# Kernel optimization log

Hardware: AMD Instinct MI355X
Metric: run time of the kernel (lower is better)

The kernel has to match this reference:

```python
import jax, jax.numpy as jnp
import numpy as np

B, N, C, H = 2, 2048, 1024, 16
D = C // H  # head_dim = 64


def _rope_freqs(n, d_half, theta=10000.0):
    inv = 1.0 / (theta ** (np.arange(0, d_half, dtype=np.float32) / d_half))
    ang = np.arange(n, dtype=np.float32)[:, None] * inv[None, :]
    return jnp.asarray(np.cos(ang)), jnp.asarray(np.sin(ang))


def setup_inputs() -> dict:
    key = jax.random.key(0)
    ks = jax.random.split(key, 5)
    cos, sin = _rope_freqs(N, D // 2)
    s = 0.02
    return {
        "x": jax.random.normal(ks[0], (B, N, C), jnp.float32),
        "w_qkv": jax.random.normal(ks[1], (3 * C, C), jnp.float32) * s,
        "b_qkv": jnp.zeros((3 * C,), jnp.float32),
        "w_proj": jax.random.normal(ks[2], (C, C), jnp.float32) * s,
        "b_proj": jnp.zeros((C,), jnp.float32),
        "freqs_cos": cos,
        "freqs_sin": sin,
    }


def _apply_rope(t, cos, sin):
    # t: (B, H, N, D); consecutive pairs (even, odd) form complex numbers,
    # matching torch.view_as_complex on reshape(..., D//2, 2).
    te = t[..., 0::2]
    to = t[..., 1::2]
    cos = cos[None, None, :, :]  # (1,1,N,D//2)
    sin = sin[None, None, :, :]
    oe = te * cos - to * sin
    oo = te * sin + to * cos
    return jnp.stack([oe, oo], axis=-1).reshape(t.shape)


def reference(x, w_qkv, b_qkv, w_proj, b_proj, freqs_cos, freqs_sin):
    b, n, c = x.shape
    qkv = x @ w_qkv.T + b_qkv                      # (B,N,3C)
    qkv = qkv.reshape(b, n, 3, H, D).transpose(2, 0, 3, 1, 4)  # (3,B,H,N,D)
    q, k, v = qkv[0], qkv[1], qkv[2]
    q = _apply_rope(q, freqs_cos, freqs_sin)
    k = _apply_rope(k, freqs_cos, freqs_sin)
    scale = 1.0 / jnp.sqrt(jnp.asarray(D, x.dtype))
    scores = jnp.einsum("bhqd,bhkd->bhqk", q, k) * scale
    attn = jax.nn.softmax(scores, axis=-1)
    out = jnp.einsum("bhqk,bhkd->bhqd", attn, v)   # (B,H,N,D)
    out = out.transpose(0, 2, 1, 3).reshape(b, n, c)
    return out @ w_proj.T + b_proj
```

## Files before the change

### kernel.cpp

```cpp
#include <hip/hip_runtime.h>
#include <hip/hip_bf16.h>
#include <stdint.h>

#define BB 2
#define NN 2048
#define CC 1024
#define HH 16
#define DD 64
#define C3 3072

typedef __attribute__((ext_vector_type(8))) short bf16x8;
typedef __attribute__((ext_vector_type(4))) float f32x4;
typedef __attribute__((ext_vector_type(4))) unsigned short ushort4_t;

__device__ __forceinline__ unsigned short f2bf(float f) {
  union { float f; unsigned u; } v; v.f = f;
  unsigned r = v.u + 0x7FFFu + ((v.u >> 16) & 1u);
  return (unsigned short)(r >> 16);
}

#if __has_builtin(__builtin_amdgcn_exp2f)
#define EXP2(x) __builtin_amdgcn_exp2f(x)
#else
#define EXP2(x) exp2f(x)
#endif

#define QSCALE 0.18033688f

#define GLDS(g, l) __builtin_amdgcn_global_load_lds( \
    (const __attribute__((address_space(1))) void*)(g), \
    (__attribute__((address_space(3))) void*)(l), 16, 0, 0)

__global__ __launch_bounds__(256) void k_cvt(
    const float* __restrict__ x, const float* __restrict__ wq,
    const float* __restrict__ wp,
    unsigned short* __restrict__ xb, unsigned short* __restrict__ wqb,
    unsigned short* __restrict__ wpb)
{
  int blk = blockIdx.x;
  const float* s; unsigned short* d; int i;
  if (blk < 4096)      { s = x;  d = xb;  i = blk * 256 + threadIdx.x; }
  else if (blk < 7168) { s = wq; d = wqb; i = (blk - 4096) * 256 + threadIdx.x; }
  else                 { s = wp; d = wpb; i = (blk - 7168) * 256 + threadIdx.x; }
  float4 v = ((const float4*)s)[i];
  ushort4_t o;
  o.x = f2bf(v.x); o.y = f2bf(v.y); o.z = f2bf(v.z); o.w = f2bf(v.w);
  ((ushort4_t*)d)[i] = o;
}

__global__ __launch_bounds__(256) void k_gemm_qkv(
    const unsigned short* __restrict__ A, const unsigned short* __restrict__ Bt,
    const float* __restrict__ bias,
    const float* __restrict__ cosb, const float* __restrict__ sinb,
    unsigned short* __restrict__ Qg, unsigned short* __restrict__ Kg,
    unsigned short* __restrict__ Vnd)
{
  __shared__ __align__(16) unsigned short As[128 * 32];
  __shared__ __align__(16) unsigned short Bs[128 * 32];
  const int tid  = threadIdx.x;
  const int lane = tid & 63;
  const int wave = tid >> 6;
  const int bm = blockIdx.y * 128;
  const int bn = blockIdx.x * 128;
  const int wm = (wave >> 1) * 64;
  const int wn = (wave & 1) * 64;
  const int frow = lane & 15;
  const int fk   = (lane >> 4) * 8;
  const int K = 1024;

  f32x4 acc[4][4] = {};

  const int row0 = tid >> 2, cc0 = tid & 3;
  const int row1 = row0 + 64;

  for (int k0 = 0; k0 < K; k0 += 32) {
    GLDS(A  + (size_t)(bm + row0) * K + k0 + cc0 * 8, As + (size_t)tid * 8);
    GLDS(Bt + (size_t)(bn + row0) * K + k0 + cc0 * 8, Bs + (size_t)tid * 8);
    GLDS(A  + (size_t)(bm + row1) * K + k0 + cc0 * 8, As + (size_t)(tid + 256) * 8);
    GLDS(Bt + (size_t)(bn + row1) * K + k0 + cc0 * 8, Bs + (size_t)(tid + 256) * 8);
    __syncthreads();

    bf16x8 af[4], bfr[4];
#pragma unroll
    for (int t = 0; t < 4; ++t) {
      af[t]  = *(const bf16x8*)(As + (wm + t * 16 + frow) * 32 + fk);
      bfr[t] = *(const bf16x8*)(Bs + (wn + t * 16 + frow) * 32 + fk);
    }
#pragma unroll
    for (int mt = 0; mt < 4; ++mt)
#pragma unroll
      for (int nt = 0; nt < 4; ++nt)
        acc[mt][nt] = __builtin_amdgcn_mfma_f32_16x16x32_bf16(af[mt], bfr[nt], acc[mt][nt], 0, 0, 0);
    __syncthreads();
  }

  const int er0  = (lane >> 4) * 4;
  const int ecol = lane & 15;
  const int region = bn >> 10;
  unsigned short* dstQK = (region == 0) ? Qg : Kg;

#pragma unroll
  for (int nt = 0; nt < 4; ++nt) {
    const int col = bn + wn + nt * 16 + ecol;
    const float bv = bias[col];
    const int c64 = (wn + nt * 16 + ecol) & 63;
    const int h   = (col >> 6) & 15;
    const int ii  = c64 >> 1;
#pragma unroll
    for (int mt = 0; mt < 4; ++mt)
#pragma unroll
      for (int r = 0; r < 4; ++r) {
        const int rowg = bm + wm + mt * 16 + er0 + r;
        const int b = rowg >> 11, n = rowg & (NN - 1);
        float v = acc[mt][nt][r] + bv;
        float vp = __shfl_xor(v, 1, 64);
        const size_t o = ((size_t)(b * HH + h) * NN + n) * DD + c64;
        if (region == 2) {
          Vnd[o] = f2bf(v);
        } else {
          float cth = cosb[n * 32 + ii], sth = sinb[n * 32 + ii];
          float ov = (c64 & 1) ? (vp * sth + v * cth)
                               : (v * cth - vp * sth);
          if (region == 0) ov *= QSCALE;
          dstQK[o] = f2bf(ov);
        }
      }
  }
}

__global__ __launch_bounds__(256) void k_vt(
    const unsigned short* __restrict__ Vnd, unsigned short* __restrict__ Vt)
{
  __shared__ unsigned short t[64][66];
  const int tid = threadIdx.x;
  const int bh = blockIdx.x >> 5;
  const int n0 = (blockIdx.x & 31) * 64;

  const unsigned short* src = Vnd + ((size_t)bh * NN + n0) * DD;
  const int nl = tid >> 2, d0 = (tid & 3) * 16;
#pragma unroll
  for (int j = 0; j < 4; ++j) {
    ushort4_t v = *(const ushort4_t*)(src + (size_t)nl * DD + d0 + j * 4);
    t[nl][d0 + j * 4 + 0] = v.x;
    t[nl][d0 + j * 4 + 1] = v.y;
    t[nl][d0 + j * 4 + 2] = v.z;
    t[nl][d0 + j * 4 + 3] = v.w;
  }
  __syncthreads();
  const int d = tid >> 2, m0 = (tid & 3) * 16;
  unsigned short* dst = Vt + ((size_t)bh * DD + d) * NN + n0 + m0;
#pragma unroll
  for (int j = 0; j < 4; ++j) {
    ushort4_t o;
    o.x = t[m0 + j * 4 + 0][d];
    o.y = t[m0 + j * 4 + 1][d];
    o.z = t[m0 + j * 4 + 2][d];
    o.w = t[m0 + j * 4 + 3][d];
    *(ushort4_t*)(dst + j * 4) = o;
  }
}

__global__ __launch_bounds__(256) void k_attn(
    const unsigned short* __restrict__ Qg, const unsigned short* __restrict__ Kg,
    const unsigned short* __restrict__ Vtg, unsigned short* __restrict__ Og)
{
  __shared__ __align__(16) unsigned short Ks[2][64 * 64];
  __shared__ __align__(16) unsigned short Vs[2][64 * 64];
  __shared__ __align__(16) unsigned short Ps[4][16 * 64];

  const int tid  = threadIdx.x;
  const int lane = tid & 63;
  const int wave = tid >> 6;
  const int bh = blockIdx.x >> 5;
  const int qt = blockIdx.x & 31;
  const int q0 = qt * 64 + wave * 16;
  const int frow   = lane & 15;
  const int fchunk = lane >> 4;
  const int er0  = (lane >> 4) * 4;
  const int ecol = lane & 15;

  const unsigned short* Qb = Qg  + (size_t)bh * NN * DD;
  const unsigned short* Kb = Kg  + (size_t)bh * NN * DD;
  const unsigned short* Vb = Vtg + (size_t)bh * DD * NN;

  bf16x8 qf[2];
#pragma unroll
  for (int kt = 0; kt < 2; ++kt)
    qf[kt] = *(const bf16x8*)(Qb + (size_t)(q0 + frow) * DD + kt * 32 + fchunk * 8);

  bf16x8 ones;
#pragma unroll
  for (int i = 0; i < 8; ++i) ones[i] = (short)0x3F80;

  f32x4 oacc[4] = {};
  f32x4 lacc = {};

  const int row0 = tid >> 3, cc0 = tid & 7;
  const int sw0 = (cc0 ^ (row0 & 7)) * 8;

  GLDS(Kb + (size_t)row0 * DD + sw0,        Ks[0] + (size_t)tid * 8);
  GLDS(Vb + (size_t)row0 * NN + sw0,        Vs[0] + (size_t)tid * 8);
  GLDS(Kb + (size_t)(row0 + 32) * DD + sw0, Ks[0] + (size_t)(tid + 256) * 8);
  GLDS(Vb + (size_t)(row0 + 32) * NN + sw0, Vs[0] + (size_t)(tid + 256) * 8);

  for (int t = 0; t < NN / 64; ++t) {
    const int p = t & 1;
    __syncthreads();

    if (t + 1 < NN / 64) {
      const int j = (t + 1) * 64;
      GLDS(Kb + (size_t)(j + row0) * DD + sw0,      Ks[1 - p] + (size_t)tid * 8);
      GLDS(Vb + (size_t)row0 * NN + j + sw0,        Vs[1 - p] + (size_t)tid * 8);
      GLDS(Kb + (size_t)(j + row0 + 32) * DD + sw0, Ks[1 - p] + (size_t)(tid + 256) * 8);
      GLDS(Vb + (size_t)(row0 + 32) * NN + j + sw0, Vs[1 - p] + (size_t)(tid + 256) * 8);
    }

    f32x4 sacc[4] = {};
#pragma unroll
    for (int nt = 0; nt < 4; ++nt) {
      int kr = nt * 16 + frow;
      bf16x8 kf0 = *(const bf16x8*)(Ks[p] + kr * 64 + ((fchunk       ^ (kr & 7)) << 3));
      bf16x8 kf1 = *(const bf16x8*)(Ks[p] + kr * 64 + (((fchunk + 4) ^ (kr & 7)) << 3));
      sacc[nt] = __builtin_amdgcn_mfma_f32_16x16x32_bf16(qf[0], kf0, sacc[nt], 0, 0, 0);
      sacc[nt] = __builtin_amdgcn_mfma_f32_16x16x32_bf16(qf[1], kf1, sacc[nt], 0, 0, 0);
    }

#pragma unroll
    for (int r = 0; r < 4; ++r) {
      int prow = er0 + r;
#pragma unroll
      for (int nt = 0; nt < 4; ++nt) {
        float pv = EXP2(sacc[nt][r]);
        union { float f; unsigned u; } cv; cv.f = pv;
        int col = nt * 16 + ecol;
        Ps[wave][prow * 64 + (((col >> 3) ^ (prow & 7)) << 3) + (col & 7)] =
            (unsigned short)(cv.u >> 16);
      }
    }

    bf16x8 pf0 = *(const bf16x8*)(&Ps[wave][frow * 64 + ((fchunk       ^ (frow & 7)) << 3)]);
    bf16x8 pf1 = *(const bf16x8*)(&Ps[wave][frow * 64 + (((fchunk + 4) ^ (frow & 7)) << 3)]);
    lacc = __builtin_amdgcn_mfma_f32_16x16x32_bf16(pf0, ones, lacc, 0, 0, 0);
    lacc = __builtin_amdgcn_mfma_f32_16x16x32_bf16(pf1, ones, lacc, 0, 0, 0);
#pragma unroll
    for (int dt = 0; dt < 4; ++dt) {
      int vr = dt * 16 + frow;
      bf16x8 vf0 = *(const bf16x8*)(Vs[p] + vr * 64 + ((fchunk       ^ (vr & 7)) << 3));
      bf16x8 vf1 = *(const bf16x8*)(Vs[p] + vr * 64 + (((fchunk + 4) ^ (vr & 7)) << 3));
      oacc[dt] = __builtin_amdgcn_mfma_f32_16x16x32_bf16(pf0, vf0, oacc[dt], 0, 0, 0);
      oacc[dt] = __builtin_amdgcn_mfma_f32_16x16x32_bf16(pf1, vf1, oacc[dt], 0, 0, 0);
    }
  }

  const int b = bh >> 4;
  const int h = bh & 15;
#pragma unroll
  for (int dt = 0; dt < 4; ++dt) {
#pragma unroll
    for (int r = 0; r < 4; ++r) {
      int qrow = q0 + er0 + r;
      int d = dt * 16 + ecol;
      float v = oacc[dt][r] / lacc[r];
      Og[(size_t)(b * NN + qrow) * CC + h * DD + d] = f2bf(v);
    }
  }
}

__global__ __launch_bounds__(256) void k_gemm_proj(
    const unsigned short* __restrict__ A, const unsigned short* __restrict__ Bt,
    const float* __restrict__ bias, float* __restrict__ Co)
{
  __shared__ __align__(16) unsigned short As[64 * 32];
  __shared__ __align__(16) unsigned short Bs[128 * 32];
  const int tid  = threadIdx.x;
  const int lane = tid & 63;
  const int wave = tid >> 6;
  const int bm = blockIdx.y * 64;
  const int bn = blockIdx.x * 128;
  const int wm = (wave >> 1) * 32;
  const int wn = (wave & 1) * 64;
  const int frow = lane & 15;
  const int fk   = (lane >> 4) * 8;
  const int K = 1024;

  f32x4 acc[2][4] = {};

  const int row0 = tid >> 2, cc0 = tid & 3;

  for (int k0 = 0; k0 < K; k0 += 32) {
    GLDS(A  + (size_t)(bm + row0) * K + k0 + cc0 * 8, As + (size_t)tid * 8);
    GLDS(Bt + (size_t)(bn + row0) * K + k0 + cc0 * 8, Bs + (size_t)tid * 8);
    GLDS(Bt + (size_t)(bn + row0 + 64) * K + k0 + cc0 * 8, Bs + (size_t)(tid + 256) * 8);
    __syncthreads();

    bf16x8 af[2], bfr[4];
#pragma unroll
    for (int t = 0; t < 2; ++t)
      af[t] = *(const bf16x8*)(As + (wm + t * 16 + frow) * 32 + fk);
#pragma unroll
    for (int t = 0; t < 4; ++t)
      bfr[t] = *(const bf16x8*)(Bs + (wn + t * 16 + frow) * 32 + fk);
#pragma unroll
    for (int mt = 0; mt < 2; ++mt)
#pragma unroll
      for (int nt = 0; nt < 4; ++nt)
        acc[mt][nt] = __builtin_amdgcn_mfma_f32_16x16x32_bf16(af[mt], bfr[nt], acc[mt][nt], 0, 0, 0);
    __syncthreads();
  }

  const int er0  = (lane >> 4) * 4;
  const int ecol = lane & 15;
#pragma unroll
  for (int nt = 0; nt < 4; ++nt) {
    int col = bn + wn + nt * 16 + ecol;
    float bv = bias[col];
#pragma unroll
    for (int mt = 0; mt < 2; ++mt)
#pragma unroll
      for (int r = 0; r < 4; ++r) {
        int rowg = bm + wm + mt * 16 + er0 + r;
        Co[(size_t)rowg * CC + col] = acc[mt][nt][r] + bv;
      }
  }
}

extern "C" void kernel_launch(void* const* d_in, const int* in_sizes, int n_in,
                              void* d_out, int out_size, void* d_ws, size_t ws_size,
                              hipStream_t stream)
{
  const float* x      = (const float*)d_in[0];
  const float* w_qkv  = (const float*)d_in[1];
  const float* b_qkv  = (const float*)d_in[2];
  const float* w_proj = (const float*)d_in[3];
  const float* b_proj = (const float*)d_in[4];
  const float* fcos   = (const float*)d_in[5];
  const float* fsin   = (const float*)d_in[6];
  float* out = (float*)d_out;

  char* ws = (char*)d_ws;
  unsigned short* xb     = (unsigned short*)(ws);
  unsigned short* wqkvb  = (unsigned short*)(ws + 8388608);
  unsigned short* wprojb = (unsigned short*)(ws + 14680064);
  unsigned short* Qb     = (unsigned short*)(ws + 16777216);
  unsigned short* Kb     = (unsigned short*)(ws + 25165824);
  unsigned short* Vnd    = (unsigned short*)(ws + 33554432);
  unsigned short* Vtb    = (unsigned short*)(ws + 41943040);
  unsigned short* aob    = (unsigned short*)(ws + 50331648);

  k_cvt<<<8192, 256, 0, stream>>>(x, w_qkv, w_proj, xb, wqkvb, wprojb);

  k_gemm_qkv<<<dim3(24, 32), 256, 0, stream>>>(xb, wqkvb, b_qkv, fcos, fsin,
                                               Qb, Kb, Vnd);
  k_vt<<<1024, 256, 0, stream>>>(Vnd, Vtb);

  k_attn<<<1024, 256, 0, stream>>>(Qb, Kb, Vtb, aob);

  k_gemm_proj<<<dim3(8, 64), 256, 0, stream>>>(aob, wprojb, b_proj, out);
}
```

Before: 218.8 us.

## Process 32 query rows per wave in attention to reuse K/V tiles

The attention kernel now gives each wave two 16-row query sub-tiles (128 queries per block), so every K and V fragment read from LDS feeds twice as many MFMAs. The grid is halved to 512 blocks and the P scratch buffer doubled. This cuts global K/V loads and LDS reads per unit of work, at the cost of more registers (accumulators doubled) and fewer blocks, which lowers occupancy and parallelism.

```diff
diff --git a/kernel.cpp b/kernel.cpp
--- a/kernel.cpp
+++ b/kernel.cpp
@@ -166,14 +166,14 @@
 {
   __shared__ __align__(16) unsigned short Ks[2][64 * 64];
   __shared__ __align__(16) unsigned short Vs[2][64 * 64];
-  __shared__ __align__(16) unsigned short Ps[4][16 * 64];
+  __shared__ __align__(16) unsigned short Ps[4][32 * 64];
 
   const int tid  = threadIdx.x;
   const int lane = tid & 63;
   const int wave = tid >> 6;
-  const int bh = blockIdx.x >> 5;
-  const int qt = blockIdx.x & 31;
-  const int q0 = qt * 64 + wave * 16;
+  const int bh = blockIdx.x >> 4;
+  const int qt = blockIdx.x & 15;
+  const int q0 = qt * 128 + wave * 32;
   const int frow   = lane & 15;
   const int fchunk = lane >> 4;
   const int er0  = (lane >> 4) * 4;
@@ -183,17 +183,19 @@
   const unsigned short* Kb = Kg  + (size_t)bh * NN * DD;
   const unsigned short* Vb = Vtg + (size_t)bh * DD * NN;
 
-  bf16x8 qf[2];
-#pragma unroll
-  for (int kt = 0; kt < 2; ++kt)
-    qf[kt] = *(const bf16x8*)(Qb + (size_t)(q0 + frow) * DD + kt * 32 + fchunk * 8);
+  bf16x8 qf[2][2];
+#pragma unroll
+  for (int m = 0; m < 2; ++m)
+#pragma unroll
+    for (int kt = 0; kt < 2; ++kt)
+      qf[m][kt] = *(const bf16x8*)(Qb + (size_t)(q0 + m * 16 + frow) * DD + kt * 32 + fchunk * 8);
 
   bf16x8 ones;
 #pragma unroll
   for (int i = 0; i < 8; ++i) ones[i] = (short)0x3F80;
 
-  f32x4 oacc[4] = {};
-  f32x4 lacc = {};
+  f32x4 oacc[2][4] = {};
+  f32x4 lacc[2] = {};
 
   const int row0 = tid >> 3, cc0 = tid & 7;
   const int sw0 = (cc0 ^ (row0 & 7)) * 8;
@@ -215,55 +217,69 @@
       GLDS(Vb + (size_t)(row0 + 32) * NN + j + sw0, Vs[1 - p] + (size_t)(tid + 256) * 8);
     }
 
-    f32x4 sacc[4] = {};
+    f32x4 sacc[2][4] = {};
 #pragma unroll
     for (int nt = 0; nt < 4; ++nt) {
       int kr = nt * 16 + frow;
       bf16x8 kf0 = *(const bf16x8*)(Ks[p] + kr * 64 + ((fchunk       ^ (kr & 7)) << 3));
       bf16x8 kf1 = *(const bf16x8*)(Ks[p] + kr * 64 + (((fchunk + 4) ^ (kr & 7)) << 3));
-      sacc[nt] = __builtin_amdgcn_mfma_f32_16x16x32_bf16(qf[0], kf0, sacc[nt], 0, 0, 0);
-      sacc[nt] = __builtin_amdgcn_mfma_f32_16x16x32_bf16(qf[1], kf1, sacc[nt], 0, 0, 0);
-    }
-
-#pragma unroll
-    for (int r = 0; r < 4; ++r) {
-      int prow = er0 + r;
-#pragma unroll
-      for (int nt = 0; nt < 4; ++nt) {
-        float pv = EXP2(sacc[nt][r]);
-        union { float f; unsigned u; } cv; cv.f = pv;
-        int col = nt * 16 + ecol;
-        Ps[wave][prow * 64 + (((col >> 3) ^ (prow & 7)) << 3) + (col & 7)] =
-            (unsigned short)(cv.u >> 16);
-      }
-    }
-
-    bf16x8 pf0 = *(const bf16x8*)(&Ps[wave][frow * 64 + ((fchunk       ^ (frow & 7)) << 3)]);
-    bf16x8 pf1 = *(const bf16x8*)(&Ps[wave][frow * 64 + (((fchunk + 4) ^ (frow & 7)) << 3)]);
-    lacc = __builtin_amdgcn_mfma_f32_16x16x32_bf16(pf0, ones, lacc, 0, 0, 0);
-    lacc = __builtin_amdgcn_mfma_f32_16x16x32_bf16(pf1, ones, lacc, 0, 0, 0);
+#pragma unroll
+      for (int m = 0; m < 2; ++m) {
+        sacc[m][nt] = __builtin_amdgcn_mfma_f32_16x16x32_bf16(qf[m][0], kf0, sacc[m][nt], 0, 0, 0);
+        sacc[m][nt] = __builtin_amdgcn_mfma_f32_16x16x32_bf16(qf[m][1], kf1, sacc[m][nt], 0, 0, 0);
+      }
+    }
+
+#pragma unroll
+    for (int m = 0; m < 2; ++m)
+#pragma unroll
+      for (int r = 0; r < 4; ++r) {
+        int prow = m * 16 + er0 + r;
+#pragma unroll
+        for (int nt = 0; nt < 4; ++nt) {
+          float pv = EXP2(sacc[m][nt][r]);
+          union { float f; unsigned u; } cv; cv.f = pv;
+          int col = nt * 16 + ecol;
+          Ps[wave][prow * 64 + (((col >> 3) ^ (prow & 7)) << 3) + (col & 7)] =
+              (unsigned short)(cv.u >> 16);
+        }
+      }
+
+    bf16x8 pf0[2], pf1[2];
+#pragma unroll
+    for (int m = 0; m < 2; ++m) {
+      int pr = m * 16 + frow;
+      pf0[m] = *(const bf16x8*)(&Ps[wave][pr * 64 + ((fchunk       ^ (pr & 7)) << 3)]);
+      pf1[m] = *(const bf16x8*)(&Ps[wave][pr * 64 + (((fchunk + 4) ^ (pr & 7)) << 3)]);
+      lacc[m] = __builtin_amdgcn_mfma_f32_16x16x32_bf16(pf0[m], ones, lacc[m], 0, 0, 0);
+      lacc[m] = __builtin_amdgcn_mfma_f32_16x16x32_bf16(pf1[m], ones, lacc[m], 0, 0, 0);
+    }
 #pragma unroll
     for (int dt = 0; dt < 4; ++dt) {
       int vr = dt * 16 + frow;
       bf16x8 vf0 = *(const bf16x8*)(Vs[p] + vr * 64 + ((fchunk       ^ (vr & 7)) << 3));
       bf16x8 vf1 = *(const bf16x8*)(Vs[p] + vr * 64 + (((fchunk + 4) ^ (vr & 7)) << 3));
-      oacc[dt] = __builtin_amdgcn_mfma_f32_16x16x32_bf16(pf0, vf0, oacc[dt], 0, 0, 0);
-      oacc[dt] = __builtin_amdgcn_mfma_f32_16x16x32_bf16(pf1, vf1, oacc[dt], 0, 0, 0);
+#pragma unroll
+      for (int m = 0; m < 2; ++m) {
+        oacc[m][dt] = __builtin_amdgcn_mfma_f32_16x16x32_bf16(pf0[m], vf0, oacc[m][dt], 0, 0, 0);
+        oacc[m][dt] = __builtin_amdgcn_mfma_f32_16x16x32_bf16(pf1[m], vf1, oacc[m][dt], 0, 0, 0);
+      }
     }
   }
 
   const int b = bh >> 4;
   const int h = bh & 15;
 #pragma unroll
-  for (int dt = 0; dt < 4; ++dt) {
-#pragma unroll
-    for (int r = 0; r < 4; ++r) {
-      int qrow = q0 + er0 + r;
-      int d = dt * 16 + ecol;
-      float v = oacc[dt][r] / lacc[r];
-      Og[(size_t)(b * NN + qrow) * CC + h * DD + d] = f2bf(v);
-    }
-  }
+  for (int m = 0; m < 2; ++m)
+#pragma unroll
+    for (int dt = 0; dt < 4; ++dt)
+#pragma unroll
+      for (int r = 0; r < 4; ++r) {
+        int qrow = q0 + m * 16 + er0 + r;
+        int d = dt * 16 + ecol;
+        float v = oacc[m][dt][r] / lacc[m][r];
+        Og[(size_t)(b * NN + qrow) * CC + h * DD + d] = f2bf(v);
+      }
 }
 
 __global__ __launch_bounds__(256) void k_gemm_proj(
@@ -353,7 +369,7 @@
                                                Qb, Kb, Vnd);
   k_vt<<<1024, 256, 0, stream>>>(Vnd, Vtb);
 
-  k_attn<<<1024, 256, 0, stream>>>(Qb, Kb, Vtb, aob);
+  k_attn<<<512, 256, 0, stream>>>(Qb, Kb, Vtb, aob);
 
   k_gemm_proj<<<dim3(8, 64), 256, 0, stream>>>(aob, wprojb, b_proj, out);
 }
```

New measurement: 226.5 us. 1.04x slower.
